# Performance work log

Measured on AMD Instinct MI355X. Metric: run time of the kernel, lower is better.

The kernel has to match this reference:

```python
import jax, jax.numpy as jnp
import numpy as np

N_HEAD = 16


def setup_inputs() -> dict:
    key = jax.random.key(0)
    k1, k2, k3 = jax.random.split(key, 3)
    B, T, C = 4, 2048, 1024
    x = jax.random.normal(k1, (B, T, C), dtype=jnp.float32)
    W = jax.random.normal(k2, (3 * C, C), dtype=jnp.float32) * (1.0 / np.sqrt(C))
    b = jax.random.normal(k3, (3 * C,), dtype=jnp.float32) * 0.02
    return {"x": x, "W": W, "b": b, "input_pos": 0}


def reference(x, W, b, input_pos):
    # cache=False path; input_pos is unused (kept for signature fidelity).
    B, T, C = x.shape
    H = N_HEAD
    hs = C // H
    # Fused QKV projection: torch Linear is x @ W.T + b -> [B, T, 3C]
    qkv = (jnp.einsum('btc,oc->bto', x, W) + b).reshape(B, T, 3, H, hs)
    # q, k, v: [B, H, T, hs]
    q = jnp.transpose(qkv[:, :, 0], (0, 2, 1, 3))
    k = jnp.transpose(qkv[:, :, 1], (0, 2, 1, 3))
    v = jnp.transpose(qkv[:, :, 2], (0, 2, 1, 3))
    scale = hs ** (-0.5)
    # scores: [B, H, T, T]
    scores = jnp.einsum('bhqd,bhkd->bhqk', q, k) * scale
    causal = jnp.tril(jnp.ones((T, T), dtype=bool))
    scores = jnp.where(causal, scores, -jnp.inf)
    wei = jax.nn.softmax(scores, axis=-1)
    out = jnp.einsum('bhqk,bhkd->bhqd', wei, v)  # [B, H, T, hs]
    return jnp.transpose(out, (0, 2, 1, 3)).reshape(B, T, C)
```

## Files before the change

### kernel.cpp

```cpp
#include <hip/hip_runtime.h>
#include <stdint.h>

using s16x8 = __attribute__((ext_vector_type(8))) short;
using u16x8 = __attribute__((ext_vector_type(8))) unsigned short;
using f32x4 = __attribute__((ext_vector_type(4))) float;

__device__ __forceinline__ unsigned short f2bf(float f) {
    union { float f; uint32_t u; } v; v.f = f;
    uint32_t u = (v.u + 0x7FFFu + ((v.u >> 16) & 1u)) >> 16;
    return (unsigned short)u;
}

__device__ __forceinline__ f32x4 zero4() { f32x4 z = {0.f, 0.f, 0.f, 0.f}; return z; }

__device__ __forceinline__ void async16(const void* g, void* l) {
    __builtin_amdgcn_global_load_lds(
        reinterpret_cast<const uint32_t __attribute__((address_space(1)))*>(
            reinterpret_cast<uintptr_t>(g)),
        reinterpret_cast<uint32_t __attribute__((address_space(3)))*>(
            (uint32_t)reinterpret_cast<uintptr_t>(l)),
        16, 0, 0);
}

__global__ void cvt_bf16(const float* __restrict__ in, unsigned short* __restrict__ out, int n) {
    int i = (blockIdx.x * 256 + threadIdx.x) * 8;
    if (i >= n) return;
    f32x4 a = *(const f32x4*)(in + i);
    f32x4 c = *(const f32x4*)(in + i + 4);
    u16x8 o;
    o[0] = f2bf(a[0]); o[1] = f2bf(a[1]); o[2] = f2bf(a[2]); o[3] = f2bf(a[3]);
    o[4] = f2bf(c[0]); o[5] = f2bf(c[1]); o[6] = f2bf(c[2]); o[7] = f2bf(c[3]);
    *(u16x8*)(out + i) = o;
}

#define SC 0.18033688011112042f

__global__ __launch_bounds__(256, 2)
void qkv_gemm(const unsigned short* __restrict__ A,
              const unsigned short* __restrict__ Bw,
              const float* __restrict__ bias,
              unsigned short* __restrict__ Qo,
              unsigned short* __restrict__ Ko,
              unsigned short* __restrict__ Vto) {
    constexpr int Kd = 1024, T = 2048, H = 16;
    __shared__ __align__(16) unsigned short As[128 * 64];
    __shared__ __align__(16) unsigned short Bs[128 * 64];
    const int tid = threadIdx.x;
    const int wave = tid >> 6, lane = tid & 63;
    const int q4 = lane >> 4, l15 = lane & 15;
    const int bm = blockIdx.y * 128, bn = blockIdx.x * 128;
    const int wm = (wave >> 1) * 64, wn = (wave & 1) * 64;

    f32x4 acc[4][4];
#pragma unroll
    for (int a = 0; a < 4; ++a)
#pragma unroll
        for (int c = 0; c < 4; ++c) acc[a][c] = zero4();

    for (int k0 = 0; k0 < Kd; k0 += 64) {
#pragma unroll
        for (int r = 0; r < 4; ++r) {
            int u = r * 256 + tid;
            int row = u >> 3, su = (u & 7) ^ (row & 7);
            async16(A + (size_t)(bm + row) * Kd + k0 + su * 8, (char*)As + u * 16);
        }
#pragma unroll
        for (int r = 0; r < 4; ++r) {
            int u = r * 256 + tid;
            int row = u >> 3, su = (u & 7) ^ (row & 7);
            async16(Bw + (size_t)(bn + row) * Kd + k0 + su * 8, (char*)Bs + u * 16);
        }
        __syncthreads();
#pragma unroll
        for (int kt = 0; kt < 2; ++kt) {
            s16x8 af[4];
#pragma unroll
            for (int mt = 0; mt < 4; ++mt) {
                int row = wm + mt * 16 + l15;
                int uu = (kt * 4 + q4) ^ (row & 7);
                af[mt] = *(const s16x8*)(As + row * 64 + uu * 8);
            }
#pragma unroll
            for (int nt = 0; nt < 4; ++nt) {
                int row = wn + nt * 16 + l15;
                int uu = (kt * 4 + q4) ^ (row & 7);
                s16x8 bfv = *(const s16x8*)(Bs + row * 64 + uu * 8);
#pragma unroll
                for (int mt = 0; mt < 4; ++mt)
                    acc[mt][nt] = __builtin_amdgcn_mfma_f32_16x16x32_bf16(af[mt], bfv, acc[mt][nt], 0, 0, 0);
            }
        }
        __syncthreads();
    }
#pragma unroll
    for (int nt = 0; nt < 4; ++nt) {
        int n = bn + wn + nt * 16 + l15;
        float bv = bias[n];
        int which = n >> 10, h = (n >> 6) & (H - 1), d = n & 63;
        if (which == 2) {
#pragma unroll
            for (int mt = 0; mt < 4; ++mt)
#pragma unroll
                for (int i = 0; i < 4; ++i) {
                    int m = bm + wm + mt * 16 + 4 * q4 + i;
                    int bb = m >> 11, t = m & (T - 1);
                    Vto[(((size_t)(bb * H + h)) * 64 + d) * T + t] = f2bf(acc[mt][nt][i] + bv);
                }
        } else {
            unsigned short* dst = (which == 0) ? Qo : Ko;
            float scl = (which == 0) ? SC : 1.0f;
#pragma unroll
            for (int mt = 0; mt < 4; ++mt)
#pragma unroll
                for (int i = 0; i < 4; ++i) {
                    int m = bm + wm + mt * 16 + 4 * q4 + i;
                    int bb = m >> 11, t = m & (T - 1);
                    dst[((((size_t)bb * H + h) * T) + t) * 64 + d] = f2bf((acc[mt][nt][i] + bv) * scl);
                }
        }
    }
}

__global__ __launch_bounds__(256, 3)
void flash_attn(const unsigned short* __restrict__ Qg,
                const unsigned short* __restrict__ Kg,
                const unsigned short* __restrict__ Vtg,
                float* __restrict__ Out) {
    constexpr int T = 2048;
    __shared__ __align__(16) unsigned short Qs[128 * 64];
    __shared__ __align__(16) unsigned short Ks[64 * 64];
    __shared__ __align__(16) unsigned short Vt[64 * 64];

    const int tid = threadIdx.x;
    const int wave = tid >> 6, lane = tid & 63;
    const int q4 = lane >> 4, l15 = lane & 15;
    const int bh = blockIdx.x;
    const int qt = (int)gridDim.y - 1 - (int)blockIdx.y;
    const int b = bh >> 4, h = bh & 15;
    const int q0 = qt * 128;
    const unsigned short* qb = Qg + (size_t)bh * T * 64;
    const unsigned short* kb = Kg + (size_t)bh * T * 64;
    const unsigned short* vtb = Vtg + (size_t)bh * 64 * T;

#pragma unroll
    for (int r = 0; r < 4; ++r) {
        int u = r * 256 + tid;
        int row = u >> 3, su = (u & 7) ^ (row & 7);
        async16(qb + (size_t)(q0 + row) * 64 + su * 8, (char*)Qs + u * 16);
    }
    __syncthreads();
    s16x8 aq[2][2];
#pragma unroll
    for (int s = 0; s < 2; ++s)
#pragma unroll
        for (int kt = 0; kt < 2; ++kt) {
            int arow = s * 64 + wave * 16 + l15;
            int au = (kt * 4 + q4) ^ (arow & 7);
            aq[s][kt] = *(const s16x8*)(Qs + arow * 64 + au * 8);
        }
    unsigned short* const Ps0 = Qs + (wave * 2 + 0) * 1024;
    unsigned short* const Ps1 = Qs + (wave * 2 + 1) * 1024;

    f32x4 oacc[2][4];
    float lsum[2][4];
#pragma unroll
    for (int s = 0; s < 2; ++s) {
#pragma unroll
        for (int ct = 0; ct < 4; ++ct) oacc[s][ct] = zero4();
#pragma unroll
        for (int i = 0; i < 4; ++i) lsum[s][i] = 0.f;
    }

    const int nkt = 2 * qt + 2;
    for (int j = 0; j < nkt; ++j) {
        const int c0 = j * 64;
#pragma unroll
        for (int r = 0; r < 2; ++r) {
            int u = r * 256 + tid;
            int row = u >> 3, su = (u & 7) ^ (row & 7);
            async16(kb + (size_t)(c0 + row) * 64 + su * 8, (char*)Ks + u * 16);
        }
#pragma unroll
        for (int r = 0; r < 2; ++r) {
            int u = r * 256 + tid;
            int row = u >> 3, su = (u & 7) ^ (row & 7);
            async16(vtb + (size_t)row * T + c0 + su * 8, (char*)Vt + u * 16);
        }
        __syncthreads();

        const bool alive0 = (j <= 2 * qt);

#pragma unroll
        for (int s = 0; s < 2; ++s) {
            if (s == 0 && !alive0) continue;
            const bool dg = (j == 2 * qt + s);
            unsigned short* const ps = (s == 0) ? Ps0 : Ps1;

            f32x4 sv[4];
#pragma unroll
            for (int t = 0; t < 4; ++t) sv[t] = zero4();
#pragma unroll
            for (int kt = 0; kt < 2; ++kt) {
#pragma unroll
                for (int t = 0; t < 4; ++t) {
                    int brow = t * 16 + l15;
                    int bu = (kt * 4 + q4) ^ (brow & 7);
                    s16x8 bk = *(const s16x8*)(Ks + brow * 64 + bu * 8);
                    sv[t] = __builtin_amdgcn_mfma_f32_16x16x32_bf16(aq[s][kt], bk, sv[t], 0, 0, 0);
                }
            }
#pragma unroll
            for (int t = 0; t < 4; ++t) {
#pragma unroll
                for (int i = 0; i < 4; ++i) {
                    float p = exp2f(sv[t][i]);
                    if (dg) {
                        int col = c0 + t * 16 + l15;
                        int row = q0 + s * 64 + wave * 16 + 4 * q4 + i;
                        if (col > row) p = 0.f;
                    }
                    lsum[s][i] += p;
                    union { float f; uint32_t u; } pb; pb.f = p;
                    int prow = 4 * q4 + i;
                    int unit = (t * 2 + (l15 >> 3)) ^ (prow & 7);
                    ps[prow * 64 + unit * 8 + (l15 & 7)] =
                        (unsigned short)((pb.u + 0x8000u) >> 16);
                }
            }
        }

#pragma unroll
        for (int kt = 0; kt < 2; ++kt) {
            int pu = ((kt * 4 + q4) ^ (l15 & 7)) * 8;
            s16x8 pa0, pa1;
            if (alive0) pa0 = *(const s16x8*)(Ps0 + l15 * 64 + pu);
            pa1 = *(const s16x8*)(Ps1 + l15 * 64 + pu);
#pragma unroll
            for (int ct = 0; ct < 4; ++ct) {
                int vrow = ct * 16 + l15;
                int vu = (kt * 4 + q4) ^ (vrow & 7);
                s16x8 vv = *(const s16x8*)(Vt + vrow * 64 + vu * 8);
                if (alive0)
                    oacc[0][ct] = __builtin_amdgcn_mfma_f32_16x16x32_bf16(pa0, vv, oacc[0][ct], 0, 0, 0);
                oacc[1][ct] = __builtin_amdgcn_mfma_f32_16x16x32_bf16(pa1, vv, oacc[1][ct], 0, 0, 0);
            }
        }
        __syncthreads();
    }
#pragma unroll
    for (int s = 0; s < 2; ++s) {
        float inv[4];
#pragma unroll
        for (int i = 0; i < 4; ++i) {
            float rs = lsum[s][i];
            rs += __shfl_xor(rs, 1, 16);
            rs += __shfl_xor(rs, 2, 16);
            rs += __shfl_xor(rs, 4, 16);
            rs += __shfl_xor(rs, 8, 16);
            inv[i] = 1.0f / rs;
        }
#pragma unroll
        for (int ct = 0; ct < 4; ++ct)
#pragma unroll
            for (int i = 0; i < 4; ++i) {
                int row = q0 + s * 64 + wave * 16 + 4 * q4 + i;
                Out[((size_t)b * T + row) * 1024 + h * 64 + ct * 16 + l15] =
                    oacc[s][ct][i] * inv[i];
            }
    }
}

extern "C" void kernel_launch(void* const* d_in, const int* in_sizes, int n_in,
                              void* d_out, int out_size, void* d_ws, size_t ws_size,
                              hipStream_t stream) {
    const float* x = (const float*)d_in[0];
    const float* W = (const float*)d_in[1];
    const float* bias = (const float*)d_in[2];
    float* out = (float*)d_out;

    unsigned short* xb = (unsigned short*)d_ws;
    unsigned short* wb = xb + 8388608;
    unsigned short* qb = wb + 3145728;
    unsigned short* kb = qb + 8388608;
    unsigned short* vtb = kb + 8388608;

    cvt_bf16<<<dim3(8388608 / 2048), dim3(256), 0, stream>>>(x, xb, 8388608);
    cvt_bf16<<<dim3(3145728 / 2048), dim3(256), 0, stream>>>(W, wb, 3145728);
    qkv_gemm<<<dim3(24, 64), dim3(256), 0, stream>>>(xb, wb, bias, qb, kb, vtb);
    flash_attn<<<dim3(64, 16), dim3(256), 0, stream>>>(qb, kb, vtb, out);
}
```

Measured before the change: 221.2 us.

## Stage V transpose through LDS and compute transposed scores for packed P stores

The QKV GEMM epilogue for V tiles now writes results into shared memory transposed, then emits 16-byte coalesced stores to the V^T buffer instead of scattered 2-byte strided stores. In attention, S is computed as K·Q^T so each lane holds four consecutive key columns for one query row. This lets P be packed and written to LDS with 8-byte stores, and it simplifies the row-sum to a two-step cross-quadrant shuffle. The cost is an extra barrier and LDS round trip in the GEMM epilogue, plus a changed register layout in the softmax path.

Result: faster. 205.1 us (-7.3%).

```diff
diff --git a/kernel.cpp b/kernel.cpp
--- a/kernel.cpp
+++ b/kernel.cpp
@@ -4,6 +4,7 @@
 using s16x8 = __attribute__((ext_vector_type(8))) short;
 using u16x8 = __attribute__((ext_vector_type(8))) unsigned short;
 using f32x4 = __attribute__((ext_vector_type(4))) float;
+using u32x2 = __attribute__((ext_vector_type(2))) uint32_t;
 
 __device__ __forceinline__ unsigned short f2bf(float f) {
     union { float f; uint32_t u; } v; v.f = f;
@@ -43,8 +44,9 @@
               unsigned short* __restrict__ Ko,
               unsigned short* __restrict__ Vto) {
     constexpr int Kd = 1024, T = 2048, H = 16;
-    __shared__ __align__(16) unsigned short As[128 * 64];
-    __shared__ __align__(16) unsigned short Bs[128 * 64];
+    __shared__ __align__(16) unsigned short smem[128 * 136];
+    unsigned short* const As = smem;
+    unsigned short* const Bs = smem + 128 * 64;
     const int tid = threadIdx.x;
     const int wave = tid >> 6, lane = tid & 63;
     const int q4 = lane >> 4, l15 = lane & 15;
@@ -92,21 +94,36 @@
         }
         __syncthreads();
     }
-#pragma unroll
-    for (int nt = 0; nt < 4; ++nt) {
-        int n = bn + wn + nt * 16 + l15;
-        float bv = bias[n];
-        int which = n >> 10, h = (n >> 6) & (H - 1), d = n & 63;
-        if (which == 2) {
+    if (bn >= 2048) {
+#pragma unroll
+        for (int nt = 0; nt < 4; ++nt) {
+            int n = bn + wn + nt * 16 + l15;
+            float bv = bias[n];
+            int dl = wn + nt * 16 + l15;
 #pragma unroll
             for (int mt = 0; mt < 4; ++mt)
 #pragma unroll
                 for (int i = 0; i < 4; ++i) {
-                    int m = bm + wm + mt * 16 + 4 * q4 + i;
-                    int bb = m >> 11, t = m & (T - 1);
-                    Vto[(((size_t)(bb * H + h)) * 64 + d) * T + t] = f2bf(acc[mt][nt][i] + bv);
+                    int ml = wm + mt * 16 + 4 * q4 + i;
+                    smem[dl * 136 + ml] = f2bf(acc[mt][nt][i] + bv);
                 }
-        } else {
+        }
+        __syncthreads();
+        const int bb = bm >> 11, t0 = bm & (T - 1);
+#pragma unroll
+        for (int rr = 0; rr < 8; ++rr) {
+            int r = wave * 32 + rr * 4 + q4;
+            int d = (bn - 2048) + r;
+            int h = d >> 6, dd = d & 63;
+            u16x8 v = *(const u16x8*)(smem + r * 136 + l15 * 8);
+            *(u16x8*)(Vto + (((size_t)(bb * H + h)) * 64 + dd) * T + t0 + l15 * 8) = v;
+        }
+    } else {
+#pragma unroll
+        for (int nt = 0; nt < 4; ++nt) {
+            int n = bn + wn + nt * 16 + l15;
+            float bv = bias[n];
+            int which = n >> 10, h = (n >> 6) & (H - 1), d = n & 63;
             unsigned short* dst = (which == 0) ? Qo : Ko;
             float scl = (which == 0) ? SC : 1.0f;
 #pragma unroll
@@ -162,14 +179,11 @@
     unsigned short* const Ps1 = Qs + (wave * 2 + 1) * 1024;
 
     f32x4 oacc[2][4];
-    float lsum[2][4];
-#pragma unroll
-    for (int s = 0; s < 2; ++s) {
+    float lsum[2] = {0.f, 0.f};
+#pragma unroll
+    for (int s = 0; s < 2; ++s)
 #pragma unroll
         for (int ct = 0; ct < 4; ++ct) oacc[s][ct] = zero4();
-#pragma unroll
-        for (int i = 0; i < 4; ++i) lsum[s][i] = 0.f;
-    }
 
     const int nkt = 2 * qt + 2;
     for (int j = 0; j < nkt; ++j) {
@@ -190,42 +204,50 @@
 
         const bool alive0 = (j <= 2 * qt);
 
+        f32x4 sv[2][4];
+#pragma unroll
+        for (int s = 0; s < 2; ++s)
+#pragma unroll
+            for (int t = 0; t < 4; ++t) sv[s][t] = zero4();
+#pragma unroll
+        for (int kt = 0; kt < 2; ++kt) {
+#pragma unroll
+            for (int t = 0; t < 4; ++t) {
+                int krow = t * 16 + l15;
+                int ku = (kt * 4 + q4) ^ (krow & 7);
+                s16x8 ak = *(const s16x8*)(Ks + krow * 64 + ku * 8);
+                sv[0][t] = __builtin_amdgcn_mfma_f32_16x16x32_bf16(ak, aq[0][kt], sv[0][t], 0, 0, 0);
+                sv[1][t] = __builtin_amdgcn_mfma_f32_16x16x32_bf16(ak, aq[1][kt], sv[1][t], 0, 0, 0);
+            }
+        }
+
 #pragma unroll
         for (int s = 0; s < 2; ++s) {
             if (s == 0 && !alive0) continue;
             const bool dg = (j == 2 * qt + s);
             unsigned short* const ps = (s == 0) ? Ps0 : Ps1;
-
-            f32x4 sv[4];
-#pragma unroll
-            for (int t = 0; t < 4; ++t) sv[t] = zero4();
-#pragma unroll
-            for (int kt = 0; kt < 2; ++kt) {
-#pragma unroll
-                for (int t = 0; t < 4; ++t) {
-                    int brow = t * 16 + l15;
-                    int bu = (kt * 4 + q4) ^ (brow & 7);
-                    s16x8 bk = *(const s16x8*)(Ks + brow * 64 + bu * 8);
-                    sv[t] = __builtin_amdgcn_mfma_f32_16x16x32_bf16(aq[s][kt], bk, sv[t], 0, 0, 0);
+            const int qrow = q0 + s * 64 + wave * 16 + l15;
+#pragma unroll
+            for (int t = 0; t < 4; ++t) {
+                float p0 = exp2f(sv[s][t][0]);
+                float p1 = exp2f(sv[s][t][1]);
+                float p2 = exp2f(sv[s][t][2]);
+                float p3 = exp2f(sv[s][t][3]);
+                if (dg) {
+                    int col = c0 + t * 16 + 4 * q4;
+                    if (col + 0 > qrow) p0 = 0.f;
+                    if (col + 1 > qrow) p1 = 0.f;
+                    if (col + 2 > qrow) p2 = 0.f;
+                    if (col + 3 > qrow) p3 = 0.f;
                 }
-            }
-#pragma unroll
-            for (int t = 0; t < 4; ++t) {
-#pragma unroll
-                for (int i = 0; i < 4; ++i) {
-                    float p = exp2f(sv[t][i]);
-                    if (dg) {
-                        int col = c0 + t * 16 + l15;
-                        int row = q0 + s * 64 + wave * 16 + 4 * q4 + i;
-                        if (col > row) p = 0.f;
-                    }
-                    lsum[s][i] += p;
-                    union { float f; uint32_t u; } pb; pb.f = p;
-                    int prow = 4 * q4 + i;
-                    int unit = (t * 2 + (l15 >> 3)) ^ (prow & 7);
-                    ps[prow * 64 + unit * 8 + (l15 & 7)] =
-                        (unsigned short)((pb.u + 0x8000u) >> 16);
-                }
+                lsum[s] += (p0 + p1) + (p2 + p3);
+                union { float f; uint32_t u; } a0, a1, a2, a3;
+                a0.f = p0; a1.f = p1; a2.f = p2; a3.f = p3;
+                u32x2 w;
+                w[0] = ((a0.u + 0x8000u) >> 16) | ((a1.u + 0x8000u) & 0xffff0000u);
+                w[1] = ((a2.u + 0x8000u) >> 16) | ((a3.u + 0x8000u) & 0xffff0000u);
+                *(u32x2*)(ps + l15 * 64 + (((2 * t + (q4 >> 1)) ^ (l15 & 7)) << 3) +
+                          ((q4 & 1) << 2)) = w;
             }
         }
 
@@ -249,16 +271,13 @@
     }
 #pragma unroll
     for (int s = 0; s < 2; ++s) {
+        float rs = lsum[s];
+        rs += __shfl_xor(rs, 16, 64);
+        rs += __shfl_xor(rs, 32, 64);
         float inv[4];
 #pragma unroll
-        for (int i = 0; i < 4; ++i) {
-            float rs = lsum[s][i];
-            rs += __shfl_xor(rs, 1, 16);
-            rs += __shfl_xor(rs, 2, 16);
-            rs += __shfl_xor(rs, 4, 16);
-            rs += __shfl_xor(rs, 8, 16);
-            inv[i] = 1.0f / rs;
-        }
+        for (int i = 0; i < 4; ++i)
+            inv[i] = 1.0f / __shfl(rs, 4 * q4 + i, 64);
 #pragma unroll
         for (int ct = 0; ct < 4; ++ct)
 #pragma unroll
```
